# Performance work log

Hardware: AMD Instinct MI355X
Metric: run time of the kernel (lower is better)

The kernel has to match this reference:

```python
import jax, jax.numpy as jnp
import numpy as np

B, S, HID = 2, 2048, 1024
NH, DK, DV = 4, 256, 256   # head_k_dim = head_v_dim = 1024 / 4
KSZ = 4                    # conv_size
EPS = 1e-5


def causal_conv1d(x, w):
    # x: [B, S, C] channels-last, w: [C, K] depthwise kernel (torch [C,1,K] squeezed)
    K = w.shape[1]
    Sn = x.shape[1]
    xp = jnp.pad(x, ((0, 0), (K - 1, 0), (0, 0)))
    # cross-correlation with left padding K-1 -> causal: out[t] = sum_j w[:,j] * x[t-(K-1)+j]
    out = xp[:, 0:Sn, :] * w[:, 0]
    for j in range(1, K):
        out = out + xp[:, j:j + Sn, :] * w[:, j]
    return out


def l2norm(x, eps=1e-6):
    return x * jax.lax.rsqrt(jnp.sum(x * x, axis=-1, keepdims=True) + eps)


def rms_norm(x, w, eps=EPS):
    return x * jax.lax.rsqrt(jnp.mean(x * x, axis=-1, keepdims=True) + eps) * w


def delta_rule(q, k, v, beta):
    # q,k: [B,S,H,dk]; v: [B,S,H,dv]; beta: [B,S,H]
    Bn, Sn, Hn, dk = q.shape
    dv = v.shape[-1]
    N = Bn * Hn
    qs = jnp.moveaxis(q, 1, 0).reshape(Sn, N, dk)
    ks = jnp.moveaxis(k, 1, 0).reshape(Sn, N, dk)
    vs = jnp.moveaxis(v, 1, 0).reshape(Sn, N, dv)
    bs = jnp.moveaxis(beta, 1, 0).reshape(Sn, N)

    S0 = jnp.zeros((N, dk, dv), q.dtype)

    def step(St, inp):
        qt, kt, vt, bt = inp
        kS = jnp.einsum('nk,nkv->nv', kt, St)              # k^T S
        St = St + jnp.einsum('nk,nv->nkv', kt, bt[:, None] * (vt - kS))
        ot = jnp.einsum('nk,nkv->nv', qt, St)
        return St, ot

    _, o = jax.lax.scan(step, S0, (qs, ks, vs, bs))        # o: [S, N, dv]
    o = o.reshape(Sn, Bn, Hn, dv)
    return jnp.moveaxis(o, 0, 1)                            # [B,S,H,dv]


def setup_inputs() -> dict:
    key = jax.random.key(0)
    ks = jax.random.split(key, 10)
    w_scale = 2.0 ** (-2.5) * np.sqrt(6.0 / (HID + HID))   # xavier_uniform with gain 2^-2.5
    u = lambda k, shp, s: jax.random.uniform(k, shp, jnp.float32, -s, s)
    return {
        'hidden_states': jax.random.normal(ks[0], (B, S, HID), jnp.float32),
        'Wq': u(ks[1], (HID, NH * DK), w_scale),
        'Wk': u(ks[2], (HID, NH * DK), w_scale),
        'Wv': u(ks[3], (HID, NH * DV), w_scale),
        'Wb': u(ks[4], (HID, NH), w_scale),
        'conv_q': jax.random.normal(ks[5], (NH * DK, KSZ), jnp.float32) * 0.2,
        'conv_k': jax.random.normal(ks[6], (NH * DK, KSZ), jnp.float32) * 0.2,
        'conv_v': jax.random.normal(ks[7], (NH * DV, KSZ), jnp.float32) * 0.2,
        'norm_w': jnp.ones((DV,), jnp.float32),
        'Wo': u(ks[8], (NH * DV, HID), w_scale),
    }


def reference(hidden_states, Wq, Wk, Wv, Wb, conv_q, conv_k, conv_v, norm_w, Wo):
    q = hidden_states @ Wq                                  # [B,S,key_dim]
    k = hidden_states @ Wk
    v = hidden_states @ Wv
    q = causal_conv1d(q, conv_q)
    k = causal_conv1d(k, conv_k)
    v = causal_conv1d(v, conv_v)
    q = jax.nn.silu(q).reshape(B, S, NH, DK)
    k = jax.nn.silu(k).reshape(B, S, NH, DK)
    v = jax.nn.silu(v).reshape(B, S, NH, DV)
    beta = jax.nn.sigmoid(hidden_states @ Wb)               # [B,S,H]
    q = l2norm(q)
    k = l2norm(k)
    o = delta_rule(q, k, v, beta)                           # [B,S,H,dv]
    o = rms_norm(o, norm_w)
    o = o.reshape(B, S, NH * DV) @ Wo                       # [B,S,HID]
    return o
```

## Files before the change

### kernel.cpp

```cpp
#include <hip/hip_runtime.h>
#include <math.h>

#define BB   2
#define SS   2048
#define HIDD 1024
#define ROWS 4096
#define NCH  32
#define CH   64

typedef unsigned short u16t;
typedef unsigned int   u32t;

typedef __attribute__((ext_vector_type(8))) short bf16x8;
typedef __attribute__((ext_vector_type(4))) float f32x4;

__device__ __forceinline__ float bf2f(u16t u) { return __uint_as_float(((u32t)u) << 16); }
__device__ __forceinline__ u16t f2bf(float f) {
    u32t b = __float_as_uint(f);
    return (u16t)((b + 0x7FFFu + ((b >> 16) & 1u)) >> 16);
}
__device__ __forceinline__ float lo_bf(u32t u) { return __uint_as_float(u << 16); }
__device__ __forceinline__ float hi_bf(u32t u) { return __uint_as_float(u & 0xFFFF0000u); }

__device__ __forceinline__ float waveReduceSum(float v) {
#pragma unroll
    for (int m = 1; m < 64; m <<= 1) v += __shfl_xor(v, m, 64);
    return v;
}

__device__ __forceinline__ void gload16(const void* g, void* l) {
    __builtin_amdgcn_global_load_lds(
        (const __attribute__((address_space(1))) unsigned int*)g,
        (__attribute__((address_space(3))) unsigned int*)l, 16, 0, 0);
}

__device__ __forceinline__ void lds_barrier() {
    asm volatile("s_waitcnt lgkmcnt(0)" ::: "memory");
    __builtin_amdgcn_s_barrier();
}

#define MFMA(a, b, c) __builtin_amdgcn_mfma_f32_16x16x32_bf16(a, b, c, 0, 0, 0)

__global__ __launch_bounds__(256) void f2bf_kernel(const float* __restrict__ in,
                                                   u16t* __restrict__ out) {
    const size_t idx = ((size_t)blockIdx.x * 256 + threadIdx.x) * 8;
    float4 a = *(const float4*)&in[idx];
    float4 b = *(const float4*)&in[idx + 4];
    ushort4 o1, o2;
    o1.x = f2bf(a.x); o1.y = f2bf(a.y); o1.z = f2bf(a.z); o1.w = f2bf(a.w);
    o2.x = f2bf(b.x); o2.y = f2bf(b.y); o2.z = f2bf(b.z); o2.w = f2bf(b.w);
    *(ushort4*)&out[idx] = o1;
    *(ushort4*)&out[idx + 4] = o2;
}

__global__ __launch_bounds__(256) void transpose_w4(const float* __restrict__ W0,
                                                    const float* __restrict__ W1,
                                                    const float* __restrict__ W2,
                                                    const float* __restrict__ W3,
                                                    u16t* __restrict__ T0,
                                                    u16t* __restrict__ T1,
                                                    u16t* __restrict__ T2,
                                                    u16t* __restrict__ T3) {
    __shared__ u16t tile[64][65];
    const int z = blockIdx.z;
    const float* W = (z == 0) ? W0 : (z == 1) ? W1 : (z == 2) ? W2 : W3;
    u16t* WT = (z == 0) ? T0 : (z == 1) ? T1 : (z == 2) ? T2 : T3;
    const int t = threadIdx.x;
    const int r0 = blockIdx.y * 64, c0 = blockIdx.x * 64;
    const int lr = t >> 2, lc4 = (t & 3) * 16;
#pragma unroll
    for (int m = 0; m < 4; ++m) {
        float4 v = *(const float4*)&W[(size_t)(r0 + lr) * 1024 + c0 + lc4 + m * 4];
        tile[lr][lc4 + m * 4 + 0] = f2bf(v.x);
        tile[lr][lc4 + m * 4 + 1] = f2bf(v.y);
        tile[lr][lc4 + m * 4 + 2] = f2bf(v.z);
        tile[lr][lc4 + m * 4 + 3] = f2bf(v.w);
    }
    __syncthreads();
#pragma unroll
    for (int m = 0; m < 16; ++m)
        WT[(size_t)(c0 + lr) * 1024 + r0 + lc4 + m] = tile[lc4 + m][lr];
}

__global__ __launch_bounds__(256) void gemm_mfma(const u16t* __restrict__ A,
                                                 const u16t* __restrict__ BT,
                                                 float* __restrict__ Cf,
                                                 u16t* __restrict__ Cb, int obf,
                                                 int M, int N, int K,
                                                 size_t bStrideP, size_t cStrideP) {
    __shared__ u16t As[128 * 64];
    __shared__ u16t Bs[128 * 64];
    const int t = threadIdx.x, l = t & 63, w = t >> 6;
    const int wr = w >> 1, wc = w & 1;
    const int rowBase = blockIdx.y * 128, colBase = blockIdx.x * 128;
    const int l15 = l & 15, g4 = l >> 4;

    const int bplane = colBase >> 10;
    const int bcol = colBase & 1023;

    const int srow = l >> 3;
    const int sj = (l & 7) ^ srow;
    const u16t* aSrc = A + (size_t)(rowBase + srow) * K + sj * 8;
    const u16t* bSrc = BT + (size_t)bplane * bStrideP + (size_t)(bcol + srow) * K + sj * 8;

    f32x4 acc[4][4];
#pragma unroll
    for (int i = 0; i < 4; ++i)
#pragma unroll
        for (int j = 0; j < 4; ++j) acc[i][j] = (f32x4){0.f, 0.f, 0.f, 0.f};

    for (int k0 = 0; k0 < K; k0 += 64) {
#pragma unroll
        for (int i = 0; i < 4; ++i) {
            const int rb = (i * 4 + w) * 8;
            gload16(aSrc + (size_t)rb * K + k0, &As[rb * 64]);
            gload16(bSrc + (size_t)rb * K + k0, &Bs[rb * 64]);
        }
        __syncthreads();
#pragma unroll
        for (int kh = 0; kh < 2; ++kh) {
            bf16x8 aF[4], bF[4];
#pragma unroll
            for (int mi = 0; mi < 4; ++mi) {
                const int row = wr * 64 + mi * 16 + l15;
                const int phys = (kh * 4 + g4) ^ (row & 7);
                aF[mi] = *(const bf16x8*)&As[row * 64 + phys * 8];
            }
#pragma unroll
            for (int ni = 0; ni < 4; ++ni) {
                const int row = wc * 64 + ni * 16 + l15;
                const int phys = (kh * 4 + g4) ^ (row & 7);
                bF[ni] = *(const bf16x8*)&Bs[row * 64 + phys * 8];
            }
#pragma unroll
            for (int mi = 0; mi < 4; ++mi)
#pragma unroll
                for (int ni = 0; ni < 4; ++ni)
                    acc[mi][ni] = MFMA(aF[mi], bF[ni], acc[mi][ni]);
        }
        __syncthreads();
    }
#pragma unroll
    for (int mi = 0; mi < 4; ++mi)
#pragma unroll
        for (int ni = 0; ni < 4; ++ni)
#pragma unroll
            for (int rg = 0; rg < 4; ++rg) {
                const int row = rowBase + wr * 64 + mi * 16 + g4 * 4 + rg;
                const int col = colBase + wc * 64 + ni * 16 + l15;
                const int plane = col >> 10, cc = col & 1023;
                const float v = acc[mi][ni][rg];
                if (obf) Cb[(size_t)plane * cStrideP + (size_t)row * 1024 + cc] = f2bf(v);
                else     Cf[(size_t)plane * cStrideP + (size_t)row * 1024 + cc] = v;
            }
}

__global__ __launch_bounds__(256) void beta_kernel(const float* __restrict__ X,
                                                   const float* __restrict__ Wb,
                                                   float* __restrict__ beta) {
    const int gw   = (blockIdx.x * blockDim.x + threadIdx.x) >> 6;
    const int lane = threadIdx.x & 63;
    if (gw >= ROWS) return;
    const float* x = X + (size_t)gw * HIDD;
    float a0 = 0.f, a1 = 0.f, a2 = 0.f, a3 = 0.f;
#pragma unroll
    for (int i = 0; i < 4; ++i) {
        const int k = lane * 16 + i * 4;
        float4 xv = *(const float4*)&x[k];
        float4 w0 = *(const float4*)&Wb[(size_t)(k + 0) * 4];
        float4 w1 = *(const float4*)&Wb[(size_t)(k + 1) * 4];
        float4 w2 = *(const float4*)&Wb[(size_t)(k + 2) * 4];
        float4 w3 = *(const float4*)&Wb[(size_t)(k + 3) * 4];
        a0 += xv.x * w0.x + xv.y * w1.x + xv.z * w2.x + xv.w * w3.x;
        a1 += xv.x * w0.y + xv.y * w1.y + xv.z * w2.y + xv.w * w3.y;
        a2 += xv.x * w0.z + xv.y * w1.z + xv.z * w2.z + xv.w * w3.z;
        a3 += xv.x * w0.w + xv.y * w1.w + xv.z * w2.w + xv.w * w3.w;
    }
    a0 = waveReduceSum(a0); a1 = waveReduceSum(a1);
    a2 = waveReduceSum(a2); a3 = waveReduceSum(a3);
    if (lane == 0) {
        float4 o = make_float4(1.f / (1.f + expf(-a0)), 1.f / (1.f + expf(-a1)),
                               1.f / (1.f + expf(-a2)), 1.f / (1.f + expf(-a3)));
        *(float4*)&beta[(size_t)gw * 4] = o;
    }
}

__global__ __launch_bounds__(256) void conv_qv(const u16t* __restrict__ inQ,
                                               const float* __restrict__ wQ,
                                               u16t* __restrict__ outQ,
                                               const u16t* __restrict__ inV,
                                               const float* __restrict__ wV,
                                               u16t* __restrict__ outV) {
    const int isQ = (blockIdx.y == 0);
    const u16t* in = isQ ? inQ : inV;
    const float* w = isQ ? wQ : wV;
    u16t* out      = isQ ? outQ : outV;
    const int doL2 = isQ;

    const int gw   = (blockIdx.x * blockDim.x + threadIdx.x) >> 6;
    const int lane = threadIdx.x & 63;
    const int r = gw >> 2;
    const int h = gw & 3;
    const int b = r >> 11;
    const int s = r & 2047;
    const int c4 = h * 256 + lane * 4;

    const float4 wr0 = *(const float4*)&w[(size_t)(c4 + 0) * 4];
    const float4 wr1 = *(const float4*)&w[(size_t)(c4 + 1) * 4];
    const float4 wr2 = *(const float4*)&w[(size_t)(c4 + 2) * 4];
    const float4 wr3 = *(const float4*)&w[(size_t)(c4 + 3) * 4];

    const size_t rowB = (size_t)(b << 11);
    float x0[4] = {0, 0, 0, 0}, x1[4] = {0, 0, 0, 0}, x2[4] = {0, 0, 0, 0}, x3[4];
    ushort4 u;
    if (s >= 3) { u = *(const ushort4*)&in[(rowB + s - 3) * HIDD + c4];
        x0[0] = bf2f(u.x); x0[1] = bf2f(u.y); x0[2] = bf2f(u.z); x0[3] = bf2f(u.w); }
    if (s >= 2) { u = *(const ushort4*)&in[(rowB + s - 2) * HIDD + c4];
        x1[0] = bf2f(u.x); x1[1] = bf2f(u.y); x1[2] = bf2f(u.z); x1[3] = bf2f(u.w); }
    if (s >= 1) { u = *(const ushort4*)&in[(rowB + s - 1) * HIDD + c4];
        x2[0] = bf2f(u.x); x2[1] = bf2f(u.y); x2[2] = bf2f(u.z); x2[3] = bf2f(u.w); }
    u = *(const ushort4*)&in[(rowB + s) * HIDD + c4];
    x3[0] = bf2f(u.x); x3[1] = bf2f(u.y); x3[2] = bf2f(u.z); x3[3] = bf2f(u.w);

    float y0 = wr0.x * x0[0] + wr0.y * x1[0] + wr0.z * x2[0] + wr0.w * x3[0];
    float y1 = wr1.x * x0[1] + wr1.y * x1[1] + wr1.z * x2[1] + wr1.w * x3[1];
    float y2 = wr2.x * x0[2] + wr2.y * x1[2] + wr2.z * x2[2] + wr2.w * x3[2];
    float y3 = wr3.x * x0[3] + wr3.y * x1[3] + wr3.z * x2[3] + wr3.w * x3[3];

    y0 = y0 / (1.f + expf(-y0)); y1 = y1 / (1.f + expf(-y1));
    y2 = y2 / (1.f + expf(-y2)); y3 = y3 / (1.f + expf(-y3));

    if (doL2) {
        float ss = y0 * y0 + y1 * y1 + y2 * y2 + y3 * y3;
        ss = waveReduceSum(ss);
        float sc = rsqrtf(ss + 1e-6f);
        y0 *= sc; y1 *= sc; y2 *= sc; y3 *= sc;
    }
    ushort4 o;
    o.x = f2bf(y0); o.y = f2bf(y1); o.z = f2bf(y2); o.w = f2bf(y3);
    *(ushort4*)&out[(size_t)r * HIDD + c4] = o;
}

__global__ __launch_bounds__(256) void conv_k_chunk(const u16t* __restrict__ pre,
                                                    const float* __restrict__ w,
                                                    u16t* __restrict__ rowout,
                                                    u16t* __restrict__ trout) {
    const int t = threadIdx.x;
    const int bh = blockIdx.x >> 5, c = blockIdx.x & 31;
    const int b = bh >> 2, h = bh & 3;
    const int i = t >> 2, g = t & 3;
    const int s = c * 64 + i;
    const size_t row = (size_t)b * 2048 + s;
    const int ch0 = h * 256 + g * 64;
    const int cloc = g * 64;
    float y[64];
#pragma unroll
    for (int m = 0; m < 8; ++m) {
        const int cm = ch0 + m * 8;
        uint4 x3 = *(const uint4*)&pre[row * 1024 + cm];
        uint4 x2 = (s >= 1) ? *(const uint4*)&pre[(row - 1) * 1024 + cm] : make_uint4(0, 0, 0, 0);
        uint4 x1 = (s >= 2) ? *(const uint4*)&pre[(row - 2) * 1024 + cm] : make_uint4(0, 0, 0, 0);
        uint4 x0 = (s >= 3) ? *(const uint4*)&pre[(row - 3) * 1024 + cm] : make_uint4(0, 0, 0, 0);
        u32t c0[4] = {x0.x, x0.y, x0.z, x0.w};
        u32t c1[4] = {x1.x, x1.y, x1.z, x1.w};
        u32t c2[4] = {x2.x, x2.y, x2.z, x2.w};
        u32t c3[4] = {x3.x, x3.y, x3.z, x3.w};
#pragma unroll
        for (int p = 0; p < 4; ++p) {
            const int ch = m * 8 + p * 2;
            float4 wA = *(const float4*)&w[(size_t)(ch0 + ch) * 4];
            float4 wB = *(const float4*)&w[(size_t)(ch0 + ch + 1) * 4];
            float ya = wA.x * lo_bf(c0[p]) + wA.y * lo_bf(c1[p]) + wA.z * lo_bf(c2[p]) + wA.w * lo_bf(c3[p]);
            float yb = wB.x * hi_bf(c0[p]) + wB.y * hi_bf(c1[p]) + wB.z * hi_bf(c2[p]) + wB.w * hi_bf(c3[p]);
            ya = ya / (1.f + expf(-ya));
            yb = yb / (1.f + expf(-yb));
            y[ch] = ya; y[ch + 1] = yb;
        }
    }
    float ss = 0.f;
#pragma unroll
    for (int e = 0; e < 64; ++e) ss += y[e] * y[e];
    ss += __shfl_xor(ss, 1);
    ss += __shfl_xor(ss, 2);
    const float sc = rsqrtf(ss + 1e-6f);
#pragma unroll
    for (int m = 0; m < 8; ++m) {
        uint4 o;
        u32t* op = (u32t*)&o;
#pragma unroll
        for (int p = 0; p < 4; ++p) {
            u16t a = f2bf(y[m * 8 + p * 2] * sc);
            u16t bb2 = f2bf(y[m * 8 + p * 2 + 1] * sc);
            op[p] = (u32t)a | ((u32t)bb2 << 16);
        }
        *(uint4*)&rowout[row * 1024 + ch0 + m * 8] = o;
    }
#pragma unroll
    for (int e = 0; e < 64; ++e)
        trout[((size_t)bh * 256 + cloc + e) * 2048 + s] = f2bf(y[e] * sc);
}

__global__ __launch_bounds__(256) void prep_kernel(const u16t* __restrict__ qcb,
                                                   const u16t* __restrict__ kcb,
                                                   const float* __restrict__ beta,
                                                   u16t* __restrict__ Tghi,
                                                   u16t* __restrict__ Tglo,
                                                   u16t* __restrict__ Agb) {
    __shared__ float KT[256][68];
    __shared__ float QT[256][68];
    __shared__ float Af[64][68];
    const int t = threadIdx.x;
    const int bhc = blockIdx.x;
    const int bh = bhc >> 5, c = bhc & 31;
    const int b = bh >> 2, h = bh & 3;
    const int tb = b * SS + c * CH;

    {
        const int i = t & 63, rb = t >> 6;
        const u16t* kg = kcb + (size_t)(tb + i) * HIDD + h * 256 + rb * 64;
        const u16t* qg = qcb + (size_t)(tb + i) * HIDD + h * 256 + rb * 64;
#pragma unroll
        for (int m = 0; m < 8; ++m) {
            uint4 kv = ((const uint4*)kg)[m];
            uint4 qv = ((const uint4*)qg)[m];
            u32t kw[4] = {kv.x, kv.y, kv.z, kv.w};
            u32t qw[4] = {qv.x, qv.y, qv.z, qv.w};
#pragma unroll
            for (int n = 0; n < 4; ++n) {
                int rr = rb * 64 + m * 8 + n * 2;
                KT[rr][i]     = lo_bf(kw[n]);
                KT[rr + 1][i] = hi_bf(kw[n]);
                QT[rr][i]     = lo_bf(qw[n]);
                QT[rr + 1][i] = hi_bf(qw[n]);
            }
        }
    }
    __syncthreads();

    const int it = t & 63, jb = t >> 6;
    float kk[16], qk[16];
#pragma unroll
    for (int m = 0; m < 16; ++m) { kk[m] = 0.f; qk[m] = 0.f; }
#pragma unroll 2
    for (int r = 0; r < 256; ++r) {
        float ki = KT[r][it];
        float qi = QT[r][it];
        float4 ka = *(const float4*)&KT[r][jb * 16 + 0];
        float4 kb = *(const float4*)&KT[r][jb * 16 + 4];
        float4 kc = *(const float4*)&KT[r][jb * 16 + 8];
        float4 kd = *(const float4*)&KT[r][jb * 16 + 12];
        float kj[16] = {ka.x, ka.y, ka.z, ka.w, kb.x, kb.y, kb.z, kb.w,
                        kc.x, kc.y, kc.z, kc.w, kd.x, kd.y, kd.z, kd.w};
#pragma unroll
        for (int m = 0; m < 16; ++m) { kk[m] += ki * kj[m]; qk[m] += qi * kj[m]; }
    }

    const float bta = beta[(size_t)(tb + it) * 4 + h];
    u16t* ag = Agb + (size_t)bhc * 4096 + (size_t)it * 64 + jb * 16;
#pragma unroll
    for (int m = 0; m < 16; ++m) {
        int j = jb * 16 + m;
        Af[it][j] = (j < it) ? bta * kk[m] : 0.f;
    }
#pragma unroll
    for (int m4 = 0; m4 < 4; ++m4) {
        ushort4 o;
        o.x = f2bf((jb * 16 + m4 * 4 + 0 <= it) ? qk[m4 * 4 + 0] : 0.f);
        o.y = f2bf((jb * 16 + m4 * 4 + 1 <= it) ? qk[m4 * 4 + 1] : 0.f);
        o.z = f2bf((jb * 16 + m4 * 4 + 2 <= it) ? qk[m4 * 4 + 2] : 0.f);
        o.w = f2bf((jb * 16 + m4 * 4 + 3 <= it) ? qk[m4 * 4 + 3] : 0.f);
        *(ushort4*)&ag[m4 * 4] = o;
    }
    __syncthreads();

    if (t < 64) {
        const int ccol = t;
        float tc[64];
#pragma unroll
        for (int j = 0; j < 64; ++j) tc[j] = (j == ccol) ? 1.f : 0.f;
#pragma unroll
        for (int i = 1; i < 64; ++i) {
            float a = 0.f;
#pragma unroll
            for (int j = 0; j < i; ++j) a += Af[i][j] * tc[j];
            tc[i] -= a;
        }
        u16t* th = Tghi + (size_t)bhc * 4096;
        u16t* tl = Tglo + (size_t)bhc * 4096;
#pragma unroll
        for (int i = 0; i < 64; ++i) {
            u16t hi = f2bf(tc[i]);
            th[i * 64 + ccol] = hi;
            tl[i * 64 + ccol] = f2bf(tc[i] - bf2f(hi));
        }
    }
}

__global__ __launch_bounds__(256, 1) void scan_mfma(const u16t* __restrict__ qcb,
                                                    const u16t* __restrict__ kcb,
                                                    const u16t* __restrict__ ktr,
                                                    const u16t* __restrict__ vcb,
                                                    const float* __restrict__ beta,
                                                    const u16t* __restrict__ TghiG,
                                                    const u16t* __restrict__ TgloG,
                                                    const u16t* __restrict__ AgbG,
                                                    u16t* __restrict__ o_raw) {
    __shared__ u16t Shi[16 * 256];
    __shared__ u16t Slo[16 * 256];
    __shared__ u16t Rhi[16 * 64];
    __shared__ u16t Rlo[16 * 64];
    __shared__ u16t Uhi[16 * 64];
    __shared__ u16t Ulo[16 * 64];

    const int t = threadIdx.x, l = t & 63, w = t >> 6;
    const int bh = blockIdx.x & 7, vt = blockIdx.x >> 3;
    const int b = bh >> 2, h = bh & 3;
    const int vcol0 = vt * 16;
    const int vlow = l & 15, g4 = l >> 4;

    for (int i = t; i < 16 * 256; i += 256) { Shi[i] = 0; Slo[i] = 0; }
    f32x4 sf[4];
#pragma unroll
    for (int q = 0; q < 4; ++q) sf[q] = (f32x4){0.f, 0.f, 0.f, 0.f};

    bf16x8 kf[8], qf[8], tfh[2], tfl[2], af[2], kcf[8];
    u16t vfb[4];
    float bta[4];

    auto loadKQ = [&](int c) {
        const size_t rb = (size_t)(b * 2048 + c * 64 + 16 * w + vlow) * 1024 + h * 256 + g4 * 8;
#pragma unroll
        for (int ks = 0; ks < 8; ++ks) {
            kf[ks] = *(const bf16x8*)(kcb + rb + ks * 32);
            qf[ks] = *(const bf16x8*)(qcb + rb + ks * 32);
        }
    };
    auto loadVB = [&](int c) {
        const int r0 = b * 2048 + c * 64 + 16 * w + 4 * g4;
#pragma unroll
        for (int rg = 0; rg < 4; ++rg) {
            vfb[rg] = vcb[(size_t)(r0 + rg) * 1024 + h * 256 + vcol0 + vlow];
            bta[rg] = beta[(size_t)(r0 + rg) * 4 + h];
        }
    };
    auto loadT = [&](int c) {
        const size_t tb2 = (size_t)(bh * 32 + c) * 4096 + (size_t)(16 * w + vlow) * 64 + g4 * 8;
        tfh[0] = *(const bf16x8*)(TghiG + tb2);
        tfh[1] = *(const bf16x8*)(TghiG + tb2 + 32);
        tfl[0] = *(const bf16x8*)(TgloG + tb2);
        tfl[1] = *(const bf16x8*)(TgloG + tb2 + 32);
    };
    auto loadA = [&](int c) {
        const size_t tb2 = (size_t)(bh * 32 + c) * 4096 + (size_t)(16 * w + vlow) * 64 + g4 * 8;
        af[0] = *(const bf16x8*)(AgbG + tb2);
        af[1] = *(const bf16x8*)(AgbG + tb2 + 32);
    };
    auto loadKC = [&](int c) {
        const size_t cb2 = ((size_t)bh * 256 + 64 * w + vlow) * 2048 + c * 64 + g4 * 8;
#pragma unroll
        for (int q2 = 0; q2 < 4; ++q2) {
            kcf[q2 * 2 + 0] = *(const bf16x8*)(ktr + cb2 + (size_t)(16 * q2) * 2048);
            kcf[q2 * 2 + 1] = *(const bf16x8*)(ktr + cb2 + (size_t)(16 * q2) * 2048 + 32);
        }
    };

    loadKQ(0); loadVB(0); loadT(0); loadA(0); loadKC(0);
    __syncthreads();

    for (int c = 0; c < NCH; ++c) {
        const int cn = (c + 1 < NCH) ? c + 1 : c;
        const int trow0 = b * 2048 + c * 64;

        f32x4 Wacc = (f32x4){0.f, 0.f, 0.f, 0.f};
        f32x4 O1   = (f32x4){0.f, 0.f, 0.f, 0.f};
#pragma unroll
        for (int ks = 0; ks < 8; ++ks) {
            const int pb = (((ks * 4 + g4) ^ (vlow & 7)) << 3);
            bf16x8 bH = *(const bf16x8*)&Shi[vlow * 256 + pb];
            bf16x8 bL = *(const bf16x8*)&Slo[vlow * 256 + pb];
            Wacc = MFMA(kf[ks], bH, Wacc); Wacc = MFMA(kf[ks], bL, Wacc);
            O1   = MFMA(qf[ks], bH, O1);   O1   = MFMA(qf[ks], bL, O1);
        }
        {
            const int tslot = 2 * w + (g4 >> 1);
            const int base = vlow * 64 + ((tslot ^ (vlow & 7)) << 3) + ((g4 & 1) << 2);
            u16t rh[4], rl[4];
#pragma unroll
            for (int rg = 0; rg < 4; ++rg) {
                float rv = bta[rg] * (bf2f(vfb[rg]) - Wacc[rg]);
                rh[rg] = f2bf(rv);
                rl[rg] = f2bf(rv - bf2f(rh[rg]));
            }
            uint2 ph, pl;
            ph.x = (u32t)rh[0] | ((u32t)rh[1] << 16); ph.y = (u32t)rh[2] | ((u32t)rh[3] << 16);
            pl.x = (u32t)rl[0] | ((u32t)rl[1] << 16); pl.y = (u32t)rl[2] | ((u32t)rl[3] << 16);
            *(uint2*)&Rhi[base] = ph;
            *(uint2*)&Rlo[base] = pl;
        }
        loadKQ(cn);
        loadVB(cn);
        __builtin_amdgcn_sched_barrier(0);
        lds_barrier();

        f32x4 Uacc = (f32x4){0.f, 0.f, 0.f, 0.f};
#pragma unroll
        for (int ks = 0; ks < 2; ++ks) {
            const int pb = (((ks * 4 + g4) ^ (vlow & 7)) << 3);
            bf16x8 bH = *(const bf16x8*)&Rhi[vlow * 64 + pb];
            bf16x8 bL = *(const bf16x8*)&Rlo[vlow * 64 + pb];
            Uacc = MFMA(tfh[ks], bH, Uacc);
            Uacc = MFMA(tfh[ks], bL, Uacc);
            Uacc = MFMA(tfl[ks], bH, Uacc);
        }
        {
            const int tslot = 2 * w + (g4 >> 1);
            const int base = vlow * 64 + ((tslot ^ (vlow & 7)) << 3) + ((g4 & 1) << 2);
            u16t uh[4], ul[4];
#pragma unroll
            for (int rg = 0; rg < 4; ++rg) {
                uh[rg] = f2bf(Uacc[rg]);
                ul[rg] = f2bf(Uacc[rg] - bf2f(uh[rg]));
            }
            uint2 ph, pl;
            ph.x = (u32t)uh[0] | ((u32t)uh[1] << 16); ph.y = (u32t)uh[2] | ((u32t)uh[3] << 16);
            pl.x = (u32t)ul[0] | ((u32t)ul[1] << 16); pl.y = (u32t)ul[2] | ((u32t)ul[3] << 16);
            *(uint2*)&Uhi[base] = ph;
            *(uint2*)&Ulo[base] = pl;
        }
        loadT(cn);
        __builtin_amdgcn_sched_barrier(0);
        lds_barrier();

        bf16x8 uhf[2], ulf[2];
#pragma unroll
        for (int ks = 0; ks < 2; ++ks) {
            const int pb = (((ks * 4 + g4) ^ (vlow & 7)) << 3);
            uhf[ks] = *(const bf16x8*)&Uhi[vlow * 64 + pb];
            ulf[ks] = *(const bf16x8*)&Ulo[vlow * 64 + pb];
        }
        f32x4 Oacc = O1;
#pragma unroll
        for (int ks = 0; ks < 2; ++ks) {
            Oacc = MFMA(af[ks], uhf[ks], Oacc);
            Oacc = MFMA(af[ks], ulf[ks], Oacc);
        }
#pragma unroll
        for (int rg = 0; rg < 4; ++rg)
            o_raw[(size_t)(trow0 + 16 * w + 4 * g4 + rg) * 1024 + h * 256 + vcol0 + vlow] = f2bf(Oacc[rg]);
        loadA(cn);

#pragma unroll
        for (int q = 0; q < 4; ++q) {
#pragma unroll
            for (int ks = 0; ks < 2; ++ks) {
                sf[q] = MFMA(kcf[q * 2 + ks], uhf[ks], sf[q]);
                sf[q] = MFMA(kcf[q * 2 + ks], ulf[ks], sf[q]);
            }
        }
        loadKC(cn);
        __builtin_amdgcn_sched_barrier(0);

#pragma unroll
        for (int q = 0; q < 4; ++q) {
            u16t sh[4], sl[4];
#pragma unroll
            for (int rg = 0; rg < 4; ++rg) {
                u16t hi = f2bf(sf[q][rg]);
                sh[rg] = hi;
                sl[rg] = f2bf(sf[q][rg] - bf2f(hi));
            }
            const int rslot = 8 * w + 2 * q + (g4 >> 1);
            const int base = vlow * 256 + ((rslot ^ (vlow & 7)) << 3) + ((g4 & 1) << 2);
            uint2 ph, pl;
            ph.x = (u32t)sh[0] | ((u32t)sh[1] << 16); ph.y = (u32t)sh[2] | ((u32t)sh[3] << 16);
            pl.x = (u32t)sl[0] | ((u32t)sl[1] << 16); pl.y = (u32t)sl[2] | ((u32t)sl[3] << 16);
            *(uint2*)&Shi[base] = ph;
            *(uint2*)&Slo[base] = pl;
        }
        lds_barrier();
    }
}

__global__ __launch_bounds__(256) void rms_kernel(const u16t* __restrict__ in,
                                                  const float* __restrict__ w,
                                                  u16t* __restrict__ out) {
    const int gw   = (blockIdx.x * blockDim.x + threadIdx.x) >> 6;
    const int lane = threadIdx.x & 63;
    const int r = gw >> 2;
    const int h = gw & 3;
    const size_t base = (size_t)r * HIDD + h * 256 + lane * 4;
    ushort4 xv = *(const ushort4*)&in[base];
    float x0 = bf2f(xv.x), x1 = bf2f(xv.y), x2 = bf2f(xv.z), x3 = bf2f(xv.w);
    float ss = x0 * x0 + x1 * x1 + x2 * x2 + x3 * x3;
    ss = waveReduceSum(ss);
    const float sc = rsqrtf(ss * (1.0f / 256.0f) + 1e-5f);
    float4 wv = *(const float4*)&w[lane * 4];
    ushort4 o;
    o.x = f2bf(x0 * sc * wv.x); o.y = f2bf(x1 * sc * wv.y);
    o.z = f2bf(x2 * sc * wv.z); o.w = f2bf(x3 * sc * wv.w);
    *(ushort4*)&out[base] = o;
}

extern "C" void kernel_launch(void* const* d_in, const int* in_sizes, int n_in,
                              void* d_out, int out_size, void* d_ws, size_t ws_size,
                              hipStream_t stream) {
    const float* X      = (const float*)d_in[0];
    const float* Wq     = (const float*)d_in[1];
    const float* Wk     = (const float*)d_in[2];
    const float* Wv     = (const float*)d_in[3];
    const float* Wb     = (const float*)d_in[4];
    const float* conv_q = (const float*)d_in[5];
    const float* conv_k = (const float*)d_in[6];
    const float* conv_v = (const float*)d_in[7];
    const float* norm_w = (const float*)d_in[8];
    const float* Wo     = (const float*)d_in[9];
    float* out = (float*)d_out;

    char* W8 = (char*)d_ws;
    const size_t MB = 1u << 20;
    u16t* Xbf   = (u16t*)(W8 + 0 * MB);
    u16t* o_raw = Xbf;
    u16t* qpre  = (u16t*)(W8 + 8 * MB);
    u16t* o_nrm = qpre;
    u16t* kpre  = (u16t*)(W8 + 16 * MB);
    u16t* Tghi  = (u16t*)(W8 + 16 * MB);
    u16t* Tglo  = (u16t*)(W8 + 18 * MB);
    u16t* Agb   = (u16t*)(W8 + 20 * MB);
    u16t* vpre  = (u16t*)(W8 + 24 * MB);
    u16t* ktr   = (u16t*)(W8 + 24 * MB);
    u16t* WqT   = (u16t*)(W8 + 32 * MB);
    u16t* qcb   = (u16t*)(W8 + 32 * MB);
    u16t* WkT   = (u16t*)(W8 + 40 * MB);
    u16t* kcb   = (u16t*)(W8 + 40 * MB);
    u16t* WvT   = (u16t*)(W8 + 48 * MB);
    u16t* vcb   = (u16t*)(W8 + 48 * MB);
    u16t* WoT   = (u16t*)(W8 + 56 * MB);
    float* betab = (float*)(W8 + 58 * MB);

    const size_t PL = 4194304;

    f2bf_kernel<<<2048, 256, 0, stream>>>(X, Xbf);
    transpose_w4<<<dim3(16, 16, 4), 256, 0, stream>>>(Wq, Wk, Wv, Wo, WqT, WkT, WvT, WoT);

    gemm_mfma<<<dim3(24, 32), 256, 0, stream>>>(Xbf, WqT, nullptr, qpre, 1,
                                                ROWS, 3072, HIDD, PL, PL);
    beta_kernel<<<ROWS / 4, 256, 0, stream>>>(X, Wb, betab);

    conv_qv<<<dim3(ROWS, 2), 256, 0, stream>>>(qpre, conv_q, qcb, vpre, conv_v, vcb);
    conv_k_chunk<<<256, 256, 0, stream>>>(kpre, conv_k, kcb, ktr);

    prep_kernel<<<256, 256, 0, stream>>>(qcb, kcb, betab, Tghi, Tglo, Agb);
    scan_mfma<<<128, 256, 0, stream>>>(qcb, kcb, ktr, vcb, betab, Tghi, Tglo, Agb, o_raw);

    rms_kernel<<<ROWS, 256, 0, stream>>>(o_raw, norm_w, o_nrm);
    gemm_mfma<<<dim3(8, 32), 256, 0, stream>>>(o_nrm, WoT, out, nullptr, 0,
                                               ROWS, HIDD, HIDD, 0, 0);
}
```

Measured before the change: 301.5 us.

## Run chunked delta-rule scan with one wavefront per block, removing barriers

The scan kernel drops from four waves per block to a single 64-lane wave that handles all 64 rows of each chunk and all 16 state tiles itself. Because only one wave touches the shared buffers, block barriers become plain LDS waitcnts. The next-chunk software prefetch of operands is removed, and each operand is loaded from global right before its MFMA. Hi/lo bf16 splitting now truncates instead of rounding to nearest, using a byte-perm pack. In exchange, each block has a quarter of the threads, fewer waves are resident to hide latency, and register pressure rises because 16 state accumulators stay live per lane.

```diff
diff --git a/kernel.cpp b/kernel.cpp
--- a/kernel.cpp
+++ b/kernel.cpp
@@ -21,6 +21,12 @@
 }
 __device__ __forceinline__ float lo_bf(u32t u) { return __uint_as_float(u << 16); }
 __device__ __forceinline__ float hi_bf(u32t u) { return __uint_as_float(u & 0xFFFF0000u); }
+__device__ __forceinline__ float truncbf(float f) {
+    return __uint_as_float(__float_as_uint(f) & 0xFFFF0000u);
+}
+__device__ __forceinline__ u32t pack_trunc2(float f0, float f1) {
+    return __builtin_amdgcn_perm(__float_as_uint(f1), __float_as_uint(f0), 0x07060302u);
+}
 
 __device__ __forceinline__ float waveReduceSum(float v) {
 #pragma unroll
@@ -32,11 +38,6 @@
     __builtin_amdgcn_global_load_lds(
         (const __attribute__((address_space(1))) unsigned int*)g,
         (__attribute__((address_space(3))) unsigned int*)l, 16, 0, 0);
-}
-
-__device__ __forceinline__ void lds_barrier() {
-    asm volatile("s_waitcnt lgkmcnt(0)" ::: "memory");
-    __builtin_amdgcn_s_barrier();
 }
 
 #define MFMA(a, b, c) __builtin_amdgcn_mfma_f32_16x16x32_bf16(a, b, c, 0, 0, 0)
@@ -396,15 +397,15 @@
     }
 }
 
-__global__ __launch_bounds__(256, 1) void scan_mfma(const u16t* __restrict__ qcb,
-                                                    const u16t* __restrict__ kcb,
-                                                    const u16t* __restrict__ ktr,
-                                                    const u16t* __restrict__ vcb,
-                                                    const float* __restrict__ beta,
-                                                    const u16t* __restrict__ TghiG,
-                                                    const u16t* __restrict__ TgloG,
-                                                    const u16t* __restrict__ AgbG,
-                                                    u16t* __restrict__ o_raw) {
+__global__ __launch_bounds__(64, 1) void scan_mfma(const u16t* __restrict__ qcb,
+                                                   const u16t* __restrict__ kcb,
+                                                   const u16t* __restrict__ ktr,
+                                                   const u16t* __restrict__ vcb,
+                                                   const float* __restrict__ beta,
+                                                   const u16t* __restrict__ TghiG,
+                                                   const u16t* __restrict__ TgloG,
+                                                   const u16t* __restrict__ AgbG,
+                                                   u16t* __restrict__ o_raw) {
     __shared__ u16t Shi[16 * 256];
     __shared__ u16t Slo[16 * 256];
     __shared__ u16t Rhi[16 * 64];
@@ -412,172 +413,140 @@
     __shared__ u16t Uhi[16 * 64];
     __shared__ u16t Ulo[16 * 64];
 
-    const int t = threadIdx.x, l = t & 63, w = t >> 6;
+    const int l = threadIdx.x;
     const int bh = blockIdx.x & 7, vt = blockIdx.x >> 3;
     const int b = bh >> 2, h = bh & 3;
     const int vcol0 = vt * 16;
     const int vlow = l & 15, g4 = l >> 4;
-
-    for (int i = t; i < 16 * 256; i += 256) { Shi[i] = 0; Slo[i] = 0; }
-    f32x4 sf[4];
-#pragma unroll
-    for (int q = 0; q < 4; ++q) sf[q] = (f32x4){0.f, 0.f, 0.f, 0.f};
-
-    bf16x8 kf[8], qf[8], tfh[2], tfl[2], af[2], kcf[8];
-    u16t vfb[4];
-    float bta[4];
-
-    auto loadKQ = [&](int c) {
-        const size_t rb = (size_t)(b * 2048 + c * 64 + 16 * w + vlow) * 1024 + h * 256 + g4 * 8;
+    const int sw = vlow & 7;
+
+    for (int i = l; i < 16 * 256; i += 64) { Shi[i] = 0; Slo[i] = 0; }
+    asm volatile("s_waitcnt lgkmcnt(0)" ::: "memory");
+
+    f32x4 sf[16];
+#pragma unroll
+    for (int q = 0; q < 16; ++q) sf[q] = (f32x4){0.f, 0.f, 0.f, 0.f};
+
+    for (int c = 0; c < NCH; ++c) {
+        const int trow0 = b * 2048 + c * 64;
+        const size_t tabase = (size_t)(bh * 32 + c) * 4096;
+
+        f32x4 Wa[4], O1[4];
+#pragma unroll
+        for (int tt = 0; tt < 4; ++tt) { Wa[tt] = (f32x4){0,0,0,0}; O1[tt] = (f32x4){0,0,0,0}; }
 #pragma unroll
         for (int ks = 0; ks < 8; ++ks) {
-            kf[ks] = *(const bf16x8*)(kcb + rb + ks * 32);
-            qf[ks] = *(const bf16x8*)(qcb + rb + ks * 32);
-        }
-    };
-    auto loadVB = [&](int c) {
-        const int r0 = b * 2048 + c * 64 + 16 * w + 4 * g4;
-#pragma unroll
-        for (int rg = 0; rg < 4; ++rg) {
-            vfb[rg] = vcb[(size_t)(r0 + rg) * 1024 + h * 256 + vcol0 + vlow];
-            bta[rg] = beta[(size_t)(r0 + rg) * 4 + h];
-        }
-    };
-    auto loadT = [&](int c) {
-        const size_t tb2 = (size_t)(bh * 32 + c) * 4096 + (size_t)(16 * w + vlow) * 64 + g4 * 8;
-        tfh[0] = *(const bf16x8*)(TghiG + tb2);
-        tfh[1] = *(const bf16x8*)(TghiG + tb2 + 32);
-        tfl[0] = *(const bf16x8*)(TgloG + tb2);
-        tfl[1] = *(const bf16x8*)(TgloG + tb2 + 32);
-    };
-    auto loadA = [&](int c) {
-        const size_t tb2 = (size_t)(bh * 32 + c) * 4096 + (size_t)(16 * w + vlow) * 64 + g4 * 8;
-        af[0] = *(const bf16x8*)(AgbG + tb2);
-        af[1] = *(const bf16x8*)(AgbG + tb2 + 32);
-    };
-    auto loadKC = [&](int c) {
-        const size_t cb2 = ((size_t)bh * 256 + 64 * w + vlow) * 2048 + c * 64 + g4 * 8;
-#pragma unroll
-        for (int q2 = 0; q2 < 4; ++q2) {
-            kcf[q2 * 2 + 0] = *(const bf16x8*)(ktr + cb2 + (size_t)(16 * q2) * 2048);
-            kcf[q2 * 2 + 1] = *(const bf16x8*)(ktr + cb2 + (size_t)(16 * q2) * 2048 + 32);
-        }
-    };
-
-    loadKQ(0); loadVB(0); loadT(0); loadA(0); loadKC(0);
-    __syncthreads();
-
-    for (int c = 0; c < NCH; ++c) {
-        const int cn = (c + 1 < NCH) ? c + 1 : c;
-        const int trow0 = b * 2048 + c * 64;
-
-        f32x4 Wacc = (f32x4){0.f, 0.f, 0.f, 0.f};
-        f32x4 O1   = (f32x4){0.f, 0.f, 0.f, 0.f};
-#pragma unroll
-        for (int ks = 0; ks < 8; ++ks) {
-            const int pb = (((ks * 4 + g4) ^ (vlow & 7)) << 3);
+            const int pb = (((ks * 4 + g4) ^ sw) << 3);
             bf16x8 bH = *(const bf16x8*)&Shi[vlow * 256 + pb];
             bf16x8 bL = *(const bf16x8*)&Slo[vlow * 256 + pb];
-            Wacc = MFMA(kf[ks], bH, Wacc); Wacc = MFMA(kf[ks], bL, Wacc);
-            O1   = MFMA(qf[ks], bH, O1);   O1   = MFMA(qf[ks], bL, O1);
-        }
-        {
-            const int tslot = 2 * w + (g4 >> 1);
-            const int base = vlow * 64 + ((tslot ^ (vlow & 7)) << 3) + ((g4 & 1) << 2);
-            u16t rh[4], rl[4];
+#pragma unroll
+            for (int tt = 0; tt < 4; ++tt) {
+                const size_t rb = (size_t)(trow0 + 16 * tt + vlow) * 1024 + h * 256 + g4 * 8 + ks * 32;
+                bf16x8 aK = *(const bf16x8*)(kcb + rb);
+                bf16x8 aQ = *(const bf16x8*)(qcb + rb);
+                Wa[tt] = MFMA(aK, bH, Wa[tt]); Wa[tt] = MFMA(aK, bL, Wa[tt]);
+                O1[tt] = MFMA(aQ, bH, O1[tt]); O1[tt] = MFMA(aQ, bL, O1[tt]);
+            }
+        }
+#pragma unroll
+        for (int tt = 0; tt < 4; ++tt) {
+            const int r0 = trow0 + 16 * tt + 4 * g4;
+            float rv[4];
 #pragma unroll
             for (int rg = 0; rg < 4; ++rg) {
-                float rv = bta[rg] * (bf2f(vfb[rg]) - Wacc[rg]);
-                rh[rg] = f2bf(rv);
-                rl[rg] = f2bf(rv - bf2f(rh[rg]));
+                float vv = bf2f(vcb[(size_t)(r0 + rg) * 1024 + h * 256 + vcol0 + vlow]);
+                float bt = beta[(size_t)(r0 + rg) * 4 + h];
+                rv[rg] = bt * (vv - Wa[tt][rg]);
             }
             uint2 ph, pl;
-            ph.x = (u32t)rh[0] | ((u32t)rh[1] << 16); ph.y = (u32t)rh[2] | ((u32t)rh[3] << 16);
-            pl.x = (u32t)rl[0] | ((u32t)rl[1] << 16); pl.y = (u32t)rl[2] | ((u32t)rl[3] << 16);
+            ph.x = pack_trunc2(rv[0], rv[1]);
+            ph.y = pack_trunc2(rv[2], rv[3]);
+            pl.x = pack_trunc2(rv[0] - truncbf(rv[0]), rv[1] - truncbf(rv[1]));
+            pl.y = pack_trunc2(rv[2] - truncbf(rv[2]), rv[3] - truncbf(rv[3]));
+            const int tslot = 2 * tt + (g4 >> 1);
+            const int base = vlow * 64 + ((tslot ^ sw) << 3) + ((g4 & 1) << 2);
             *(uint2*)&Rhi[base] = ph;
             *(uint2*)&Rlo[base] = pl;
         }
-        loadKQ(cn);
-        loadVB(cn);
+        asm volatile("s_waitcnt lgkmcnt(0)" ::: "memory");
         __builtin_amdgcn_sched_barrier(0);
-        lds_barrier();
-
-        f32x4 Uacc = (f32x4){0.f, 0.f, 0.f, 0.f};
+
+        f32x4 Ua[4];
+#pragma unroll
+        for (int tt = 0; tt < 4; ++tt) Ua[tt] = (f32x4){0,0,0,0};
 #pragma unroll
         for (int ks = 0; ks < 2; ++ks) {
-            const int pb = (((ks * 4 + g4) ^ (vlow & 7)) << 3);
+            const int pb = (((ks * 4 + g4) ^ sw) << 3);
             bf16x8 bH = *(const bf16x8*)&Rhi[vlow * 64 + pb];
             bf16x8 bL = *(const bf16x8*)&Rlo[vlow * 64 + pb];
-            Uacc = MFMA(tfh[ks], bH, Uacc);
-            Uacc = MFMA(tfh[ks], bL, Uacc);
-            Uacc = MFMA(tfl[ks], bH, Uacc);
-        }
-        {
-            const int tslot = 2 * w + (g4 >> 1);
-            const int base = vlow * 64 + ((tslot ^ (vlow & 7)) << 3) + ((g4 & 1) << 2);
-            u16t uh[4], ul[4];
-#pragma unroll
-            for (int rg = 0; rg < 4; ++rg) {
-                uh[rg] = f2bf(Uacc[rg]);
-                ul[rg] = f2bf(Uacc[rg] - bf2f(uh[rg]));
-            }
+#pragma unroll
+            for (int tt = 0; tt < 4; ++tt) {
+                const size_t tb2 = tabase + (size_t)(16 * tt + vlow) * 64 + g4 * 8 + ks * 32;
+                bf16x8 tH = *(const bf16x8*)(TghiG + tb2);
+                bf16x8 tL = *(const bf16x8*)(TgloG + tb2);
+                Ua[tt] = MFMA(tH, bH, Ua[tt]);
+                Ua[tt] = MFMA(tH, bL, Ua[tt]);
+                Ua[tt] = MFMA(tL, bH, Ua[tt]);
+            }
+        }
+#pragma unroll
+        for (int tt = 0; tt < 4; ++tt) {
             uint2 ph, pl;
-            ph.x = (u32t)uh[0] | ((u32t)uh[1] << 16); ph.y = (u32t)uh[2] | ((u32t)uh[3] << 16);
-            pl.x = (u32t)ul[0] | ((u32t)ul[1] << 16); pl.y = (u32t)ul[2] | ((u32t)ul[3] << 16);
+            ph.x = pack_trunc2(Ua[tt][0], Ua[tt][1]);
+            ph.y = pack_trunc2(Ua[tt][2], Ua[tt][3]);
+            pl.x = pack_trunc2(Ua[tt][0] - truncbf(Ua[tt][0]), Ua[tt][1] - truncbf(Ua[tt][1]));
+            pl.y = pack_trunc2(Ua[tt][2] - truncbf(Ua[tt][2]), Ua[tt][3] - truncbf(Ua[tt][3]));
+            const int tslot = 2 * tt + (g4 >> 1);
+            const int base = vlow * 64 + ((tslot ^ sw) << 3) + ((g4 & 1) << 2);
             *(uint2*)&Uhi[base] = ph;
             *(uint2*)&Ulo[base] = pl;
         }
-        loadT(cn);
+        asm volatile("s_waitcnt lgkmcnt(0)" ::: "memory");
         __builtin_amdgcn_sched_barrier(0);
-        lds_barrier();
 
         bf16x8 uhf[2], ulf[2];
 #pragma unroll
         for (int ks = 0; ks < 2; ++ks) {
-            const int pb = (((ks * 4 + g4) ^ (vlow & 7)) << 3);
+            const int pb = (((ks * 4 + g4) ^ sw) << 3);
             uhf[ks] = *(const bf16x8*)&Uhi[vlow * 64 + pb];
             ulf[ks] = *(const bf16x8*)&Ulo[vlow * 64 + pb];
         }
-        f32x4 Oacc = O1;
-#pragma unroll
-        for (int ks = 0; ks < 2; ++ks) {
-            Oacc = MFMA(af[ks], uhf[ks], Oacc);
-            Oacc = MFMA(af[ks], ulf[ks], Oacc);
-        }
-#pragma unroll
-        for (int rg = 0; rg < 4; ++rg)
-            o_raw[(size_t)(trow0 + 16 * w + 4 * g4 + rg) * 1024 + h * 256 + vcol0 + vlow] = f2bf(Oacc[rg]);
-        loadA(cn);
-
-#pragma unroll
-        for (int q = 0; q < 4; ++q) {
+#pragma unroll
+        for (int tt = 0; tt < 4; ++tt) {
+            f32x4 Oa = O1[tt];
 #pragma unroll
             for (int ks = 0; ks < 2; ++ks) {
-                sf[q] = MFMA(kcf[q * 2 + ks], uhf[ks], sf[q]);
-                sf[q] = MFMA(kcf[q * 2 + ks], ulf[ks], sf[q]);
-            }
-        }
-        loadKC(cn);
-        __builtin_amdgcn_sched_barrier(0);
-
-#pragma unroll
-        for (int q = 0; q < 4; ++q) {
-            u16t sh[4], sl[4];
-#pragma unroll
-            for (int rg = 0; rg < 4; ++rg) {
-                u16t hi = f2bf(sf[q][rg]);
-                sh[rg] = hi;
-                sl[rg] = f2bf(sf[q][rg] - bf2f(hi));
-            }
-            const int rslot = 8 * w + 2 * q + (g4 >> 1);
-            const int base = vlow * 256 + ((rslot ^ (vlow & 7)) << 3) + ((g4 & 1) << 2);
+                const size_t tb2 = tabase + (size_t)(16 * tt + vlow) * 64 + g4 * 8 + ks * 32;
+                bf16x8 aA = *(const bf16x8*)(AgbG + tb2);
+                Oa = MFMA(aA, uhf[ks], Oa);
+                Oa = MFMA(aA, ulf[ks], Oa);
+            }
+#pragma unroll
+            for (int rg = 0; rg < 4; ++rg)
+                o_raw[(size_t)(trow0 + 16 * tt + 4 * g4 + rg) * 1024 + h * 256 + vcol0 + vlow] = f2bf(Oa[rg]);
+        }
+#pragma unroll
+        for (int q = 0; q < 16; ++q) {
+            const size_t cb2 = ((size_t)bh * 256 + 16 * q + vlow) * 2048 + c * 64 + g4 * 8;
+            bf16x8 k0 = *(const bf16x8*)(ktr + cb2);
+            bf16x8 k1 = *(const bf16x8*)(ktr + cb2 + 32);
+            sf[q] = MFMA(k0, uhf[0], sf[q]); sf[q] = MFMA(k0, ulf[0], sf[q]);
+            sf[q] = MFMA(k1, uhf[1], sf[q]); sf[q] = MFMA(k1, ulf[1], sf[q]);
+        }
+#pragma unroll
+        for (int q = 0; q < 16; ++q) {
             uint2 ph, pl;
-            ph.x = (u32t)sh[0] | ((u32t)sh[1] << 16); ph.y = (u32t)sh[2] | ((u32t)sh[3] << 16);
-            pl.x = (u32t)sl[0] | ((u32t)sl[1] << 16); pl.y = (u32t)sl[2] | ((u32t)sl[3] << 16);
+            ph.x = pack_trunc2(sf[q][0], sf[q][1]);
+            ph.y = pack_trunc2(sf[q][2], sf[q][3]);
+            pl.x = pack_trunc2(sf[q][0] - truncbf(sf[q][0]), sf[q][1] - truncbf(sf[q][1]));
+            pl.y = pack_trunc2(sf[q][2] - truncbf(sf[q][2]), sf[q][3] - truncbf(sf[q][3]));
+            const int rslot = 2 * q + (g4 >> 1);
+            const int base = vlow * 256 + ((rslot ^ sw) << 3) + ((g4 & 1) << 2);
             *(uint2*)&Shi[base] = ph;
             *(uint2*)&Slo[base] = pl;
         }
-        lds_barrier();
+        asm volatile("s_waitcnt lgkmcnt(0)" ::: "memory");
+        __builtin_amdgcn_sched_barrier(0);
     }
 }
 
@@ -650,7 +619,7 @@
     conv_k_chunk<<<256, 256, 0, stream>>>(kpre, conv_k, kcb, ktr);
 
     prep_kernel<<<256, 256, 0, stream>>>(qcb, kcb, betab, Tghi, Tglo, Agb);
-    scan_mfma<<<128, 256, 0, stream>>>(qcb, kcb, ktr, vcb, betab, Tghi, Tglo, Agb, o_raw);
+    scan_mfma<<<128, 64, 0, stream>>>(qcb, kcb, ktr, vcb, betab, Tghi, Tglo, Agb, o_raw);
 
     rms_kernel<<<ROWS, 256, 0, stream>>>(o_raw, norm_w, o_nrm);
     gemm_mfma<<<dim3(8, 32), 256, 0, stream>>>(o_nrm, WoT, out, nullptr, 0,
```

Measured after the change: 799.5 us. +165.2%, slower.
